# Optimization experiments

Measured on AMD Instinct MI355X. Metric: run time of the kernel, lower is better.

Reference implementation:

```python
import jax, jax.numpy as jnp
import numpy as np

DIM = 1024
HEADS = 16
DIM_HEAD = 64
INNER = HEADS * DIM_HEAD  # 1024
SCALE = DIM_HEAD ** (-0.5)
EPS = 1e-5


def _layernorm(x, g, b):
    mu = jnp.mean(x, axis=-1, keepdims=True)
    var = jnp.mean(jnp.square(x - mu), axis=-1, keepdims=True)
    return (x - mu) * jax.lax.rsqrt(var + EPS) * g + b


def _split_heads(t):
    # b t n (h d) -> b h t n d
    b, T, n, _ = t.shape
    return t.reshape(b, T, n, HEADS, DIM_HEAD).transpose(0, 3, 1, 2, 4)


def setup_inputs() -> dict:
    key = jax.random.key(0)
    ks = jax.random.split(key, 9)
    b, T, n1, n2 = 8, 4, 1024, 64
    x = jax.random.normal(ks[0], (b, T, n1, DIM), dtype=jnp.float32)
    latents = jax.random.normal(ks[1], (b, T, n2, DIM), dtype=jnp.float32)
    g_media = 1.0 + 0.02 * jax.random.normal(ks[2], (DIM,), dtype=jnp.float32)
    b_media = 0.02 * jax.random.normal(ks[3], (DIM,), dtype=jnp.float32)
    g_lat = 1.0 + 0.02 * jax.random.normal(ks[4], (DIM,), dtype=jnp.float32)
    b_lat = 0.02 * jax.random.normal(ks[5], (DIM,), dtype=jnp.float32)
    s = DIM ** (-0.5)
    Wq = jax.random.normal(ks[6], (DIM, INNER), dtype=jnp.float32) * s
    Wkv = jax.random.normal(ks[7], (DIM, 2 * INNER), dtype=jnp.float32) * s
    Wo = jax.random.normal(ks[8], (INNER, DIM), dtype=jnp.float32) * (INNER ** (-0.5))
    return {"x": x, "latents": latents, "g_media": g_media, "b_media": b_media,
            "g_lat": g_lat, "b_lat": b_lat, "Wq": Wq, "Wkv": Wkv, "Wo": Wo}


def reference(x, latents, g_media, b_media, g_lat, b_lat, Wq, Wkv, Wo):
    x = _layernorm(x, g_media, b_media)          # (b, T, n1, D)
    lat = _layernorm(latents, g_lat, b_lat)      # (b, T, n2, D)

    q = lat @ Wq                                 # (b, T, n2, inner)
    kv_input = jnp.concatenate((x, lat), axis=-2)  # (b, T, n1+n2, D)
    kv = kv_input @ Wkv                          # (b, T, n1+n2, 2*inner)
    k, v = jnp.split(kv, 2, axis=-1)

    q = _split_heads(q) * SCALE                  # (b, h, T, n2, d)
    k = _split_heads(k)                          # (b, h, T, n1+n2, d)
    v = _split_heads(v)

    sim = jnp.einsum('bhtid,bhtjd->bhtij', q, k)  # (b, h, T, n2, n1+n2)
    attn = jax.nn.softmax(sim, axis=-1)           # stable (amax subtracted)
    out = jnp.einsum('bhtij,bhtjd->bhtid', attn, v)

    # b h t n d -> b t n (h d)
    b, h, T, n, d = out.shape
    out = out.transpose(0, 2, 3, 1, 4).reshape(b, T, n, h * d)
    return out @ Wo
```

## Files before the change

### kernel.cpp

```cpp
#include <hip/hip_runtime.h>

#define DEVI __device__ __forceinline__

typedef unsigned short u16;
typedef unsigned int u32;

using bf16x8 = __attribute__((ext_vector_type(8))) short;
using f32x4  = __attribute__((ext_vector_type(4))) float;

DEVI u16 f2bf(float f) {
  u32 u = __builtin_bit_cast(u32, f);
  u32 r = (u + 0x7fffu + ((u >> 16) & 1u)) >> 16;
  return (u16)r;
}

DEVI void gl_lds16(const u16* g, u16* l) {
  __builtin_amdgcn_global_load_lds(
      (const __attribute__((address_space(1))) u32*)g,
      (__attribute__((address_space(3))) u32*)l, 16, 0, 0);
}

__global__ __launch_bounds__(256) void ln_kernel(
    const float* __restrict__ x, const float* __restrict__ lat,
    const float* __restrict__ gm, const float* __restrict__ bm,
    const float* __restrict__ gl, const float* __restrict__ bl,
    u16* __restrict__ kvin, u16* __restrict__ latb)
{
  int row = blockIdx.x;
  int bt = row / 1088, r = row % 1088;
  const float *src, *g, *b;
  bool is_lat = (r >= 1024);
  if (!is_lat) { src = x + ((size_t)bt*1024 + r)*1024; g = gm; b = bm; }
  else         { src = lat + ((size_t)bt*64 + (r-1024))*1024; g = gl; b = bl; }
  int tid = threadIdx.x;
  float4 v = *(const float4*)(src + tid*4);
  float s1 = v.x+v.y+v.z+v.w;
  float s2 = v.x*v.x+v.y*v.y+v.z*v.z+v.w*v.w;
  for (int off=32; off; off>>=1){ s1 += __shfl_down(s1,off); s2 += __shfl_down(s2,off); }
  __shared__ float red[2][4];
  int w = tid>>6, lane = tid&63;
  if (lane==0){ red[0][w]=s1; red[1][w]=s2; }
  __syncthreads();
  s1 = red[0][0]+red[0][1]+red[0][2]+red[0][3];
  s2 = red[1][0]+red[1][1]+red[1][2]+red[1][3];
  float mu = s1 * (1.f/1024.f);
  float var = s2 * (1.f/1024.f) - mu*mu;
  float rstd = rsqrtf(var + 1e-5f);
  float4 gv = *(const float4*)(g + tid*4);
  float4 bv = *(const float4*)(b + tid*4);
  ushort4 o;
  o.x = f2bf((v.x-mu)*rstd*gv.x + bv.x);
  o.y = f2bf((v.y-mu)*rstd*gv.y + bv.y);
  o.z = f2bf((v.z-mu)*rstd*gv.z + bv.z);
  o.w = f2bf((v.w-mu)*rstd*gv.w + bv.w);
  *(ushort4*)(kvin + (size_t)row*1024 + tid*4) = o;
  if (is_lat) *(ushort4*)(latb + ((size_t)(bt*64 + (r-1024)))*1024 + tid*4) = o;
}

__global__ __launch_bounds__(256) void transpose_cast(
    const float* __restrict__ in, u16* __restrict__ out, int R, int C)
{
  __shared__ float t[32][33];
  int bx = blockIdx.x*32, by = blockIdx.y*32;
  int tx = threadIdx.x & 31, ty = threadIdx.x >> 5;
  for (int k=0;k<32;k+=8) t[ty+k][tx] = in[(size_t)(by+ty+k)*C + bx+tx];
  __syncthreads();
  for (int k=0;k<32;k+=8) out[(size_t)(bx+ty+k)*R + by+tx] = f2bf(t[tx][ty+k]);
}

__global__ __launch_bounds__(256,2) void gemm_bt_f32(
    const u16* __restrict__ A, const u16* __restrict__ BT,
    float* __restrict__ C, int N, int K)
{
  __shared__ u16 lA[128*32];
  __shared__ u16 lB[128*32];
  int tid = threadIdx.x;
  int w = tid>>6, lane = tid&63;
  int li = lane&15, lg = lane>>4;
  int m0 = blockIdx.y*128, n0 = blockIdx.x*128;
  int wr = (w>>1)*64, wc = (w&1)*64;
  f32x4 acc[4][4] = {};
  int sr = lane>>2;
  int sk = ((lane&3) ^ ((lane>>3)&3))*8;
  const int rchunk = (lg ^ ((li>>1)&3))*8;
  const u16* pa = A  + (size_t)(m0 + w*32 + sr)*K + sk;
  const u16* pb = BT + (size_t)(n0 + w*32 + sr)*K + sk;
  u16* la0 = lA + (w*2)*512; u16* la1 = lA + (w*2+1)*512;
  u16* lb0 = lB + (w*2)*512; u16* lb1 = lB + (w*2+1)*512;
  for (int k0=0; k0<K; k0+=32) {
    gl_lds16(pa,        la0);
    gl_lds16(pa + 16*(size_t)K, la1);
    gl_lds16(pb,        lb0);
    gl_lds16(pb + 16*(size_t)K, lb1);
    pa += 32; pb += 32;
    __syncthreads();
    bf16x8 af[4], bfr[4];
    #pragma unroll
    for (int m=0;m<4;++m) af[m]  = *(const bf16x8*)(lA + (wr + m*16 + li)*32 + rchunk);
    #pragma unroll
    for (int n=0;n<4;++n) bfr[n] = *(const bf16x8*)(lB + (wc + n*16 + li)*32 + rchunk);
    #pragma unroll
    for (int m=0;m<4;++m)
      #pragma unroll
      for (int n=0;n<4;++n)
        acc[m][n] = __builtin_amdgcn_mfma_f32_16x16x32_bf16(af[m], bfr[n], acc[m][n], 0,0,0);
    __syncthreads();
  }
  #pragma unroll
  for (int m=0;m<4;++m)
    #pragma unroll
    for (int n=0;n<4;++n) {
      int row = m0 + wr + m*16 + lg*4;
      int col = n0 + wc + n*16 + li;
      #pragma unroll
      for (int rg=0;rg<4;++rg)
        C[(size_t)(row+rg)*N + col] = acc[m][n][rg];
    }
}

__global__ __launch_bounds__(512,2) void gemm256_kvq(
    const u16* __restrict__ A, const u16* __restrict__ BT,
    const u16* __restrict__ Aq, const u16* __restrict__ BTq,
    u16* __restrict__ kb, u16* __restrict__ vt, u16* __restrict__ qb)
{
  __shared__ u16 lds[2][2][2][256][32];
  const int tid = threadIdx.x;
  const int w = tid>>6, lane = tid&63;
  const int li = lane&15, lg = lane>>4;
  const int wm = w>>2, wn = w&3;
  const int bid = blockIdx.x;
  const int swz = (bid&7)*140 + (bid>>3);
  const bool is_q = (swz >= 1088);
  const u16* Asrc; const u16* Bsrc; int m0, n0;
  if (!is_q) { Asrc = A;  Bsrc = BT;  m0 = (swz>>3)*256;        n0 = (swz&7)*256; }
  else       { int qt = swz-1088; Asrc = Aq; Bsrc = BTq; m0 = (qt>>2)*256; n0 = (qt&3)*256; }
  const int srow = lane>>2;
  const int scol = ((lane&3) ^ ((lane>>3)&3))*8;
  const int rchunk = (lg ^ ((li>>1)&3))*8;

#define STAGE(b, mat, kh, kt) do {                                            \
    const u16* _s = (mat) ? Bsrc : Asrc;                                      \
    const int _base = (mat) ? n0 : m0;                                        \
    _Pragma("unroll")                                                         \
    for (int L=0; L<2; ++L) {                                                 \
      const int _r = L*128 + w*16;                                            \
      gl_lds16(_s + (size_t)(_base + _r + srow)*1024 + (kt)*64 + (kh)*32 + scol, \
               &lds[b][mat][kh][_r][0]);                                      \
    }                                                                         \
  } while(0)

  f32x4 acc[8][4] = {};

  STAGE(0,0,0,0); STAGE(0,1,0,0); STAGE(0,0,1,0); STAGE(0,1,1,0);
  asm volatile("s_waitcnt vmcnt(4) lgkmcnt(0)\n\ts_barrier" ::: "memory");

  for (int j=0; j<16; ++j) {
    const int c = j&1;
    const int kt = (j<15) ? j+1 : 15;
    STAGE(c^1,0,0,kt); STAGE(c^1,1,0,kt);
    {
      bf16x8 a0[8], b0[4];
      #pragma unroll
      for (int mf=0; mf<8; ++mf)
        a0[mf] = *(const bf16x8*)&lds[c][0][0][wm*128 + mf*16 + li][rchunk];
      #pragma unroll
      for (int nf=0; nf<4; ++nf)
        b0[nf] = *(const bf16x8*)&lds[c][1][0][wn*64 + nf*16 + li][rchunk];
      __builtin_amdgcn_s_setprio(1);
      #pragma unroll
      for (int mf=0; mf<8; ++mf)
        #pragma unroll
        for (int nf=0; nf<4; ++nf)
          acc[mf][nf] = __builtin_amdgcn_mfma_f32_16x16x32_bf16(a0[mf], b0[nf], acc[mf][nf], 0,0,0);
      __builtin_amdgcn_s_setprio(0);
    }
    asm volatile("s_waitcnt vmcnt(4) lgkmcnt(0)\n\ts_barrier" ::: "memory");
    STAGE(c^1,0,1,kt); STAGE(c^1,1,1,kt);
    {
      bf16x8 a1[8], b1[4];
      #pragma unroll
      for (int mf=0; mf<8; ++mf)
        a1[mf] = *(const bf16x8*)&lds[c][0][1][wm*128 + mf*16 + li][rchunk];
      #pragma unroll
      for (int nf=0; nf<4; ++nf)
        b1[nf] = *(const bf16x8*)&lds[c][1][1][wn*64 + nf*16 + li][rchunk];
      __builtin_amdgcn_s_setprio(1);
      #pragma unroll
      for (int mf=0; mf<8; ++mf)
        #pragma unroll
        for (int nf=0; nf<4; ++nf)
          acc[mf][nf] = __builtin_amdgcn_mfma_f32_16x16x32_bf16(a1[mf], b1[nf], acc[mf][nf], 0,0,0);
      __builtin_amdgcn_s_setprio(0);
    }
    asm volatile("s_waitcnt vmcnt(4) lgkmcnt(0)\n\ts_barrier" ::: "memory");
  }
#undef STAGE

  if (is_q) {
    #pragma unroll
    for (int am=0; am<8; ++am)
      #pragma unroll
      for (int nf=0; nf<4; ++nf) {
        int row = m0 + wm*128 + am*16 + lg*4;
        int col = n0 + wn*64 + nf*16 + li;
        #pragma unroll
        for (int rg=0; rg<4; ++rg)
          qb[(size_t)(row+rg)*1024 + col] = f2bf(acc[am][nf][rg]*0.125f);
      }
  } else if (n0 < 1024) {
    #pragma unroll
    for (int am=0; am<8; ++am)
      #pragma unroll
      for (int nf=0; nf<4; ++nf) {
        int row = m0 + wm*128 + am*16 + lg*4;
        int col = n0 + wn*64 + nf*16 + li;
        #pragma unroll
        for (int rg=0; rg<4; ++rg)
          kb[(size_t)(row+rg)*1024 + col] = f2bf(acc[am][nf][rg]);
      }
  } else {
    #pragma unroll
    for (int am=0; am<8; ++am)
      #pragma unroll
      for (int nf=0; nf<4; ++nf) {
        int r0 = m0 + wm*128 + am*16 + lg*4;
        int cc = n0 + wn*64 + nf*16 + li - 1024;
        int bt = r0/1088, jj = r0 - bt*1088;
        ushort4 o;
        o.x = f2bf(acc[am][nf][0]); o.y = f2bf(acc[am][nf][1]);
        o.z = f2bf(acc[am][nf][2]); o.w = f2bf(acc[am][nf][3]);
        *(ushort4*)(vt + ((size_t)(bt*1024 + cc))*1088 + jj) = o;
      }
  }
}

__global__ __launch_bounds__(256,2) void attn_kernel(
    const u16* __restrict__ qbuf, const u16* __restrict__ kbuf,
    const u16* __restrict__ vT, u16* __restrict__ aout)
{
  __shared__ u16 p_im[4][16][72];
  int blk = blockIdx.x;
  int bt = blk >> 4, h = blk & 15;
  int w = threadIdx.x>>6, lane = threadIdx.x&63;
  int li = lane&15, lg = lane>>4;
  const u16* qrow = qbuf + ((size_t)(bt*64 + w*16 + li))*1024 + h*64;
  bf16x8 qf0 = *(const bf16x8*)(qrow + lg*8);
  bf16x8 qf1 = *(const bf16x8*)(qrow + 32 + lg*8);
  float mrun = -INFINITY, lrun = 0.f;
  f32x4 oacc[4] = {};
  const u16* kbase = kbuf + (size_t)bt*1088*1024 + h*64;
  const u16* vbase = vT + ((size_t)(bt*1024 + h*64))*1088;
  for (int c=0; c<17; ++c) {
    int j0 = c*64;
    f32x4 s[4] = {};
    #pragma unroll
    for (int jt=0; jt<4; ++jt) {
      const u16* krow = kbase + (size_t)(j0 + jt*16 + li)*1024;
      bf16x8 k0 = *(const bf16x8*)(krow + lg*8);
      bf16x8 k1 = *(const bf16x8*)(krow + 32 + lg*8);
      s[jt] = __builtin_amdgcn_mfma_f32_16x16x32_bf16(k0, qf0, s[jt], 0,0,0);
      s[jt] = __builtin_amdgcn_mfma_f32_16x16x32_bf16(k1, qf1, s[jt], 0,0,0);
    }
    float cm = -INFINITY;
    #pragma unroll
    for (int jt=0;jt<4;++jt)
      cm = fmaxf(cm, fmaxf(fmaxf(s[jt][0], s[jt][1]), fmaxf(s[jt][2], s[jt][3])));
    cm = fmaxf(cm, __shfl_xor(cm,16));
    cm = fmaxf(cm, __shfl_xor(cm,32));
    float mnew = fmaxf(mrun, cm);
    float sf = __expf(mrun - mnew);
    float ls = 0.f;
    #pragma unroll
    for (int jt=0;jt<4;++jt) {
      float p0 = __expf(s[jt][0]-mnew), p1 = __expf(s[jt][1]-mnew);
      float p2 = __expf(s[jt][2]-mnew), p3 = __expf(s[jt][3]-mnew);
      ls += p0+p1+p2+p3;
      ushort4 pk; pk.x = f2bf(p0); pk.y = f2bf(p1); pk.z = f2bf(p2); pk.w = f2bf(p3);
      *(ushort4*)&p_im[w][li][jt*16 + lg*4] = pk;
    }
    ls += __shfl_xor(ls,16);
    ls += __shfl_xor(ls,32);
    lrun = lrun*sf + ls;
    mrun = mnew;
    float sfr[4];
    #pragma unroll
    for (int rg=0;rg<4;++rg) sfr[rg] = __shfl(sf, lg*4+rg);
    #pragma unroll
    for (int dt=0;dt<4;++dt) {
      oacc[dt][0]*=sfr[0]; oacc[dt][1]*=sfr[1]; oacc[dt][2]*=sfr[2]; oacc[dt][3]*=sfr[3];
    }
    bf16x8 pa0 = *(const bf16x8*)&p_im[w][li][lg*8];
    bf16x8 pa1 = *(const bf16x8*)&p_im[w][li][32 + lg*8];
    #pragma unroll
    for (int dt=0;dt<4;++dt) {
      const u16* vrow = vbase + (size_t)(dt*16 + li)*1088 + j0;
      bf16x8 v0 = *(const bf16x8*)(vrow + lg*8);
      bf16x8 v1 = *(const bf16x8*)(vrow + 32 + lg*8);
      oacc[dt] = __builtin_amdgcn_mfma_f32_16x16x32_bf16(pa0, v0, oacc[dt], 0,0,0);
      oacc[dt] = __builtin_amdgcn_mfma_f32_16x16x32_bf16(pa1, v1, oacc[dt], 0,0,0);
    }
  }
  float linv[4];
  #pragma unroll
  for (int rg=0;rg<4;++rg) linv[rg] = 1.f / __shfl(lrun, lg*4+rg);
  u16* orow = aout + ((size_t)(bt*64 + w*16))*1024 + h*64;
  #pragma unroll
  for (int dt=0;dt<4;++dt)
    #pragma unroll
    for (int rg=0;rg<4;++rg)
      orow[(size_t)(lg*4+rg)*1024 + dt*16 + li] = f2bf(oacc[dt][rg]*linv[rg]);
}

extern "C" void kernel_launch(void* const* d_in, const int* in_sizes, int n_in,
                              void* d_out, int out_size, void* d_ws, size_t ws_size,
                              hipStream_t stream) {
  const float* x   = (const float*)d_in[0];
  const float* lat = (const float*)d_in[1];
  const float* gm  = (const float*)d_in[2];
  const float* bm  = (const float*)d_in[3];
  const float* gl  = (const float*)d_in[4];
  const float* bl  = (const float*)d_in[5];
  const float* Wq  = (const float*)d_in[6];
  const float* Wkv = (const float*)d_in[7];
  const float* Wo  = (const float*)d_in[8];
  float* out = (float*)d_out;

  char* ws = (char*)d_ws;
  const size_t KV_BYTES = (size_t)32*1088*1024*2;
  u16* kvin = (u16*)(ws);
  u16* kbuf = (u16*)(ws + KV_BYTES);
  u16* vT   = (u16*)(ws + 2*KV_BYTES);
  u16* latb = (u16*)(ws + 3*KV_BYTES);
  u16* qbuf = (u16*)(ws + 3*KV_BYTES + (size_t)4194304);
  u16* aout = (u16*)(ws + 3*KV_BYTES + (size_t)2*4194304);
  u16* wqT  = (u16*)(ws + 3*KV_BYTES + (size_t)3*4194304);
  u16* wkvT = (u16*)(ws + 3*KV_BYTES + (size_t)3*4194304 + 2097152);
  u16* woT  = (u16*)(ws + 3*KV_BYTES + (size_t)3*4194304 + 2097152 + 4194304);

  ln_kernel<<<dim3(32*1088), dim3(256), 0, stream>>>(x, lat, gm, bm, gl, bl, kvin, latb);
  transpose_cast<<<dim3(32,32), dim3(256), 0, stream>>>(Wq,  wqT,  1024, 1024);
  transpose_cast<<<dim3(64,32), dim3(256), 0, stream>>>(Wkv, wkvT, 1024, 2048);
  transpose_cast<<<dim3(32,32), dim3(256), 0, stream>>>(Wo,  woT,  1024, 1024);

  gemm256_kvq<<<dim3(1120), dim3(512), 0, stream>>>(kvin, wkvT, latb, wqT, kbuf, vT, qbuf);
  attn_kernel<<<dim3(512), dim3(256), 0, stream>>>(qbuf, kbuf, vT, aout);
  gemm_bt_f32<<<dim3(8,16), dim3(256), 0, stream>>>(aout, woT, out, 1024, 1024);
}
```

Measured before the change: 304.9 us.

## Split GEMM k-loop into four interleaved phases with finer barriers

Restructures the projection GEMM main loop into four sub-phases per k-tile. Each phase loads half of the A fragments from LDS, issues one STAGE of global-to-LDS loads, then runs 16 MFMAs, with barriers placed between phases. This is a ping-pong style schedule meant to overlap LDS reads and global loads with matrix math and to lower register pressure by holding only four A fragments at a time. The cost is more barriers per iteration and tighter synchronisation ordering.

```diff
diff --git a/kernel.cpp b/kernel.cpp
--- a/kernel.cpp
+++ b/kernel.cpp
@@ -148,53 +148,89 @@
                &lds[b][mat][kh][_r][0]);                                      \
     }                                                                         \
   } while(0)
+#define BARRIER() asm volatile("s_barrier" ::: "memory")
+#define LGKM0()   do { asm volatile("s_waitcnt lgkmcnt(0)" ::: "memory"); \
+                       __builtin_amdgcn_sched_barrier(0); } while(0)
+#define VM4()     asm volatile("s_waitcnt vmcnt(4)" ::: "memory")
 
   f32x4 acc[8][4] = {};
 
   STAGE(0,0,0,0); STAGE(0,1,0,0); STAGE(0,0,1,0); STAGE(0,1,1,0);
-  asm volatile("s_waitcnt vmcnt(4) lgkmcnt(0)\n\ts_barrier" ::: "memory");
+  VM4(); BARRIER();
 
   for (int j=0; j<16; ++j) {
     const int c = j&1;
     const int kt = (j<15) ? j+1 : 15;
-    STAGE(c^1,0,0,kt); STAGE(c^1,1,0,kt);
-    {
-      bf16x8 a0[8], b0[4];
-      #pragma unroll
-      for (int mf=0; mf<8; ++mf)
-        a0[mf] = *(const bf16x8*)&lds[c][0][0][wm*128 + mf*16 + li][rchunk];
+    bf16x8 a[4], b0[4], b1[4];
+
+    #pragma unroll
+    for (int mf=0; mf<4; ++mf)
+      a[mf] = *(const bf16x8*)&lds[c][0][0][wm*128 + mf*16 + li][rchunk];
+    #pragma unroll
+    for (int nf=0; nf<4; ++nf)
+      b0[nf] = *(const bf16x8*)&lds[c][1][0][wn*64 + nf*16 + li][rchunk];
+    STAGE(c^1,0,0,kt);
+    BARRIER(); LGKM0();
+    __builtin_amdgcn_s_setprio(1);
+    #pragma unroll
+    for (int mf=0; mf<4; ++mf)
       #pragma unroll
       for (int nf=0; nf<4; ++nf)
-        b0[nf] = *(const bf16x8*)&lds[c][1][0][wn*64 + nf*16 + li][rchunk];
-      __builtin_amdgcn_s_setprio(1);
-      #pragma unroll
-      for (int mf=0; mf<8; ++mf)
-        #pragma unroll
-        for (int nf=0; nf<4; ++nf)
-          acc[mf][nf] = __builtin_amdgcn_mfma_f32_16x16x32_bf16(a0[mf], b0[nf], acc[mf][nf], 0,0,0);
-      __builtin_amdgcn_s_setprio(0);
-    }
-    asm volatile("s_waitcnt vmcnt(4) lgkmcnt(0)\n\ts_barrier" ::: "memory");
-    STAGE(c^1,0,1,kt); STAGE(c^1,1,1,kt);
-    {
-      bf16x8 a1[8], b1[4];
-      #pragma unroll
-      for (int mf=0; mf<8; ++mf)
-        a1[mf] = *(const bf16x8*)&lds[c][0][1][wm*128 + mf*16 + li][rchunk];
+        acc[mf][nf] = __builtin_amdgcn_mfma_f32_16x16x32_bf16(a[mf], b0[nf], acc[mf][nf], 0,0,0);
+    __builtin_amdgcn_s_setprio(0);
+    BARRIER();
+
+    #pragma unroll
+    for (int mf=0; mf<4; ++mf)
+      a[mf] = *(const bf16x8*)&lds[c][0][0][wm*128 + 64 + mf*16 + li][rchunk];
+    STAGE(c^1,1,0,kt);
+    VM4();
+    BARRIER(); LGKM0();
+    __builtin_amdgcn_s_setprio(1);
+    #pragma unroll
+    for (int mf=0; mf<4; ++mf)
       #pragma unroll
       for (int nf=0; nf<4; ++nf)
-        b1[nf] = *(const bf16x8*)&lds[c][1][1][wn*64 + nf*16 + li][rchunk];
-      __builtin_amdgcn_s_setprio(1);
-      #pragma unroll
-      for (int mf=0; mf<8; ++mf)
-        #pragma unroll
-        for (int nf=0; nf<4; ++nf)
-          acc[mf][nf] = __builtin_amdgcn_mfma_f32_16x16x32_bf16(a1[mf], b1[nf], acc[mf][nf], 0,0,0);
-      __builtin_amdgcn_s_setprio(0);
-    }
-    asm volatile("s_waitcnt vmcnt(4) lgkmcnt(0)\n\ts_barrier" ::: "memory");
+        acc[4+mf][nf] = __builtin_amdgcn_mfma_f32_16x16x32_bf16(a[mf], b0[nf], acc[4+mf][nf], 0,0,0);
+    __builtin_amdgcn_s_setprio(0);
+    BARRIER();
+
+    #pragma unroll
+    for (int mf=0; mf<4; ++mf)
+      a[mf] = *(const bf16x8*)&lds[c][0][1][wm*128 + mf*16 + li][rchunk];
+    #pragma unroll
+    for (int nf=0; nf<4; ++nf)
+      b1[nf] = *(const bf16x8*)&lds[c][1][1][wn*64 + nf*16 + li][rchunk];
+    STAGE(c^1,0,1,kt);
+    BARRIER(); LGKM0();
+    __builtin_amdgcn_s_setprio(1);
+    #pragma unroll
+    for (int mf=0; mf<4; ++mf)
+      #pragma unroll
+      for (int nf=0; nf<4; ++nf)
+        acc[mf][nf] = __builtin_amdgcn_mfma_f32_16x16x32_bf16(a[mf], b1[nf], acc[mf][nf], 0,0,0);
+    __builtin_amdgcn_s_setprio(0);
+    BARRIER();
+
+    #pragma unroll
+    for (int mf=0; mf<4; ++mf)
+      a[mf] = *(const bf16x8*)&lds[c][0][1][wm*128 + 64 + mf*16 + li][rchunk];
+    STAGE(c^1,1,1,kt);
+    VM4();
+    BARRIER(); LGKM0();
+    __builtin_amdgcn_s_setprio(1);
+    #pragma unroll
+    for (int mf=0; mf<4; ++mf)
+      #pragma unroll
+      for (int nf=0; nf<4; ++nf)
+        acc[4+mf][nf] = __builtin_amdgcn_mfma_f32_16x16x32_bf16(a[mf], b1[nf], acc[4+mf][nf], 0,0,0);
+    __builtin_amdgcn_s_setprio(0);
+    BARRIER();
   }
 #undef STAGE
+#undef BARRIER
+#undef LGKM0
+#undef VM4
 
   if (is_q) {
     #pragma unroll
```

Result: no change. 303.6 us (-0.4%).
